# Performance work log

Hardware: AMD Instinct MI355X
Metric: run time of the kernel (lower is better)

## Reference

```python
import jax, jax.numpy as jnp
import numpy as np

B, C, N = 4, 128, 25000
E = 200000            # edges per graph
H, DH = 4, 32         # heads, per-head dim
OUT = H * DH          # 128
ED = 32               # edge feature dim


def setup_inputs() -> dict:
    key = jax.random.key(0)
    ks = jax.random.split(key, 16)
    s = 0.05
    return {
        'x': jax.random.normal(ks[0], (B, C, N, 1), jnp.float32),
        'edge_index': jax.random.randint(ks[1], (B, 2, E), 0, B * N, jnp.int64),
        'edge_attr': jax.random.normal(ks[2], (B * E, ED), jnp.float32),
        'Wq': jax.random.normal(ks[3], (C, OUT), jnp.float32) * s,
        'bq': jnp.zeros((OUT,), jnp.float32),
        'Wk': jax.random.normal(ks[4], (C, OUT), jnp.float32) * s,
        'bk': jnp.zeros((OUT,), jnp.float32),
        'Wv': jax.random.normal(ks[5], (C, OUT), jnp.float32) * s,
        'bv': jnp.zeros((OUT,), jnp.float32),
        'We': jax.random.normal(ks[6], (ED, OUT), jnp.float32) * s,
        'Wskip': jax.random.normal(ks[7], (C, OUT), jnp.float32) * s,
        'bskip': jnp.zeros((OUT,), jnp.float32),
        'W1': jax.random.normal(ks[8], (OUT, 2 * OUT), jnp.float32) * s,
        'b1': jnp.zeros((2 * OUT,), jnp.float32),
        'W2': jax.random.normal(ks[9], (2 * OUT, OUT), jnp.float32) * s,
        'b2': jnp.zeros((OUT,), jnp.float32),
    }


def reference(x, edge_index, edge_attr, Wq, bq, Wk, bk, Wv, bv, We,
              Wskip, bskip, W1, b1, W2, b2):
    b, c, n, _ = x.shape
    nb = b * n
    # [B,C,N,1] -> [B*N, C]
    xf = x.squeeze(-1).transpose(0, 2, 1).reshape(nb, c)
    # [B,2,E] -> [2, B*E]
    ei = edge_index.transpose(1, 0, 2).reshape(2, -1)
    src, dst = ei[0], ei[1]

    q = (xf @ Wq + bq).reshape(nb, H, DH)
    k = (xf @ Wk + bk).reshape(nb, H, DH)
    v = (xf @ Wv + bv).reshape(nb, H, DH)
    e = (edge_attr @ We).reshape(-1, H, DH)  # [T,H,DH]

    qi = q[dst]            # gather target queries  [T,H,DH]
    kj = k[src] + e        # gather source keys + edge proj
    vj = v[src] + e

    scale = 1.0 / np.sqrt(DH).astype(np.float32)
    alpha = (qi * kj).sum(-1) * scale  # [T,H]

    # segment softmax over edges sharing a destination node
    amax = jax.ops.segment_max(alpha, dst, num_segments=nb)
    amax = jnp.where(jnp.isfinite(amax), amax, 0.0)
    ea = jnp.exp(alpha - amax[dst])
    denom = jax.ops.segment_sum(ea, dst, num_segments=nb)
    attn = ea / (denom[dst] + 1e-16)   # [T,H]

    agg = jax.ops.segment_sum(vj * attn[..., None], dst, num_segments=nb)
    out = agg.reshape(nb, OUT) + (xf @ Wskip + bskip)  # root skip

    # feed-forward + final activation
    h = jnp.maximum(out @ W1 + b1, 0.0) @ W2 + b2
    h = jnp.maximum(h, 0.0)

    # [B*N, OUT] -> [B, OUT, N, 1]
    return h.reshape(b, n, OUT).transpose(0, 2, 1)[..., None]
```

## Files before the change

### kernel.cpp

```cpp
#include <hip/hip_runtime.h>
#include <hip/hip_bf16.h>

#define NB      100000
#define NPB     25000
#define T_E     800000
#define EPG     200000
#define DMODEL  128
#define EDIM    32
#define FFD     256
#define SCAN_NBLK 98

typedef __attribute__((ext_vector_type(8))) short bf16x8;
typedef __attribute__((ext_vector_type(4))) float f32x4;
typedef __attribute__((ext_vector_type(2))) float f32x2;

__device__ inline unsigned short f2bf(float f) {
    unsigned u = __float_as_uint(f);
    unsigned r = u + 0x7fffu + ((u >> 16) & 1u);
    return (unsigned short)(r >> 16);
}
__device__ inline unsigned pack_bf16x2(float lo, float hi) {
    return (unsigned)f2bf(lo) | ((unsigned)f2bf(hi) << 16);
}
__device__ inline float bf_lo(unsigned p) { return __uint_as_float(p << 16); }
__device__ inline float bf_hi(unsigned p) { return __uint_as_float(p & 0xffff0000u); }

__global__ __launch_bounds__(256) void k_prep(
    const float* __restrict__ W1, const float* __restrict__ W2,
    const float* __restrict__ We,
    const float* __restrict__ Wq, const float* __restrict__ Wk,
    const float* __restrict__ Wv, const float* __restrict__ Wskip,
    uint4* __restrict__ w1f, uint4* __restrict__ w2f,
    uint4* __restrict__ wef, uint4* __restrict__ wpf)
{
    int t = blockIdx.x * 256 + threadIdx.x;
    int lane = t & 63;
    int frag = t >> 6;
    if (frag >= 264) return;
    int rl = lane & 15, g = lane >> 4;
    unsigned v[4];
    if (frag < 64) {
        int m1 = frag >> 2, ks = frag & 3;
        int col1 = m1 * 16 + rl;
        int k0 = ks * 32 + g * 8;
#pragma unroll
        for (int j2 = 0; j2 < 4; ++j2) {
            float f0 = W1[(k0 + 2 * j2) * FFD + col1];
            float f1 = W1[(k0 + 2 * j2 + 1) * FFD + col1];
            v[j2] = pack_bf16x2(f0, f1);
        }
        w1f[frag * 64 + lane] = make_uint4(v[0], v[1], v[2], v[3]);
    } else if (frag < 128) {
        int f2 = frag - 64;
        int m2 = f2 >> 3, ks = f2 & 7;
        int c2 = m2 * 16 + rl;
        int k0 = ks * 32 + g * 8;
#pragma unroll
        for (int j2 = 0; j2 < 4; ++j2) {
            float f0 = W2[(k0 + 2 * j2) * DMODEL + c2];
            float f1 = W2[(k0 + 2 * j2 + 1) * DMODEL + c2];
            v[j2] = pack_bf16x2(f0, f1);
        }
        w2f[f2 * 64 + lane] = make_uint4(v[0], v[1], v[2], v[3]);
    } else if (frag < 136) {
        int m = frag - 128;
        int ocol = m * 16 + rl;
        int k0 = g * 8;
#pragma unroll
        for (int j2 = 0; j2 < 4; ++j2) {
            float f0 = We[(k0 + 2 * j2) * DMODEL + ocol];
            float f1 = We[(k0 + 2 * j2 + 1) * DMODEL + ocol];
            v[j2] = pack_bf16x2(f0, f1);
        }
        wef[m * 64 + lane] = make_uint4(v[0], v[1], v[2], v[3]);
    } else {
        int fi = frag - 136;
        int m  = fi >> 5;
        int r  = fi & 31;
        int ct = r >> 2, ks = r & 3;
        const float* W = (m == 0) ? Wq : (m == 1) ? Wk : (m == 2) ? Wv : Wskip;
        int col = ct * 16 + rl;
        int k0  = ks * 32 + g * 8;
#pragma unroll
        for (int j2 = 0; j2 < 4; ++j2) {
            float f0 = W[(k0 + 2 * j2) * DMODEL + col];
            float f1 = W[(k0 + 2 * j2 + 1) * DMODEL + col];
            v[j2] = pack_bf16x2(f0, f1);
        }
        wpf[fi * 64 + lane] = make_uint4(v[0], v[1], v[2], v[3]);
    }
}

__global__ __launch_bounds__(256) void k_proj2(
    const float* __restrict__ x, const uint4* __restrict__ wpf,
    const float* __restrict__ bq, const float* __restrict__ bk,
    const float* __restrict__ bv, const float* __restrict__ bskip,
    unsigned short* __restrict__ qb16, unsigned short* __restrict__ kvb,
    unsigned short* __restrict__ skipb16)
{
    __shared__ __align__(16) char lds[16384];
    const int tid   = threadIdx.x;
    const int node0 = blockIdx.x * 64;

    {
        const int nl   = tid & 63;
        const int half = tid >> 6;
        const int node = node0 + nl;
        const bool valid = node < NB;
        int b  = node / NPB;
        int nn = node - b * NPB;
        const float* xbase = x + (size_t)b * DMODEL * NPB + nn;
#pragma unroll
        for (int o = 0; o < 4; ++o) {
            int c0 = (half * 4 + o) * 8;
            unsigned vals[4];
#pragma unroll
            for (int j2 = 0; j2 < 4; ++j2) {
                float f0 = valid ? xbase[(size_t)(c0 + 2 * j2) * NPB] : 0.f;
                float f1 = valid ? xbase[(size_t)(c0 + 2 * j2 + 1) * NPB] : 0.f;
                vals[j2] = pack_bf16x2(f0, f1);
            }
            int byte = nl * 256 + ((c0 * 2) ^ ((nl & 7) << 4));
            *(uint4*)(&lds[byte]) = make_uint4(vals[0], vals[1], vals[2], vals[3]);
        }
    }
    __syncthreads();

    const int w = tid >> 6, lane = tid & 63;
    const int rl = lane & 15, g = lane >> 4;

    const uint4* wf = wpf + (size_t)w * 32 * 64;
    const float* bi = (w == 0) ? bq : (w == 1) ? bk : (w == 2) ? bv : bskip;
    unsigned short* base = (w == 0) ? qb16 : (w == 3) ? skipb16
                          : kvb + ((w == 2) ? 128 : 0);
    const int rowstride = (w == 1 || w == 2) ? 256 : 128;

#pragma unroll
    for (int ct = 0; ct < 8; ++ct) {
        bf16x8 A[4];
#pragma unroll
        for (int ks = 0; ks < 4; ++ks)
            A[ks] = *(const bf16x8*)&wf[(ct * 4 + ks) * 64 + lane];
        const int colb = ct * 16 + g * 4;
        const float bb0 = bi[colb], bb1 = bi[colb + 1],
                    bb2 = bi[colb + 2], bb3 = bi[colb + 3];
#pragma unroll
        for (int nt = 0; nt < 4; ++nt) {
            const int nl = nt * 16 + rl;
            f32x4 acc = {0.f, 0.f, 0.f, 0.f};
#pragma unroll
            for (int ks = 0; ks < 4; ++ks) {
                bf16x8 B = *(const bf16x8*)(&lds[nl * 256 +
                              ((ks * 64 + g * 16) ^ ((nl & 7) << 4))]);
                acc = __builtin_amdgcn_mfma_f32_16x16x32_bf16(A[ks], B, acc, 0, 0, 0);
            }
            const int node = node0 + nl;
            if (node < NB) {
                unsigned lo = pack_bf16x2(acc[0] + bb0, acc[1] + bb1);
                unsigned hi = pack_bf16x2(acc[2] + bb2, acc[3] + bb3);
                *(uint2*)&base[(size_t)node * rowstride + colb] = make_uint2(lo, hi);
            }
        }
    }
}

__global__ __launch_bounds__(256) void k_hist(
    const int* __restrict__ eidx, int* __restrict__ counts)
{
    int t = blockIdx.x * 256 + threadIdx.x;
    if (t < T_E) {
        int b = t / EPG, e = t - b * EPG;
        int dst = eidx[(size_t)(b * 2 + 1) * EPG + e];
        atomicAdd(&counts[dst], 1);
    }
}

__global__ __launch_bounds__(1024) void k_scan1(
    const int* __restrict__ counts, int* __restrict__ row_start,
    int* __restrict__ bsum)
{
    __shared__ int s[1024];
    const int tid = threadIdx.x;
    const int gid = blockIdx.x * 1024 + tid;
    int v = (gid < NB) ? counts[gid] : 0;
    s[tid] = v;
    __syncthreads();
#pragma unroll
    for (int off = 1; off < 1024; off <<= 1) {
        int tv = (tid >= off) ? s[tid - off] : 0;
        __syncthreads();
        s[tid] += tv;
        __syncthreads();
    }
    int incl = s[tid];
    if (gid < NB) row_start[gid] = incl - v;
    if (tid == 1023) bsum[blockIdx.x] = incl;
}

__global__ __launch_bounds__(128) void k_scan2(int* __restrict__ bsum)
{
    __shared__ int s[128];
    const int tid = threadIdx.x;
    int v = (tid < SCAN_NBLK) ? bsum[tid] : 0;
    s[tid] = v;
    __syncthreads();
#pragma unroll
    for (int off = 1; off < 128; off <<= 1) {
        int tv = (tid >= off) ? s[tid - off] : 0;
        __syncthreads();
        s[tid] += tv;
        __syncthreads();
    }
    if (tid < SCAN_NBLK) bsum[tid] = s[tid] - v;
}

__global__ __launch_bounds__(1024) void k_scan3(
    int* __restrict__ row_start, const int* __restrict__ bsum,
    int* __restrict__ cursor)
{
    const int gid = blockIdx.x * 1024 + threadIdx.x;
    if (gid < NB) {
        int v = row_start[gid] + bsum[blockIdx.x];
        row_start[gid] = v;
        cursor[gid] = v;
    }
}

__global__ __launch_bounds__(256) void k_scatter(
    const int* __restrict__ eidx, int* __restrict__ cursor,
    int2* __restrict__ elist2)
{
    int t = blockIdx.x * 256 + threadIdx.x;
    if (t < T_E) {
        int b = t / EPG, e = t - b * EPG;
        int dst = eidx[(size_t)(b * 2 + 1) * EPG + e];
        int src = eidx[(size_t)(b * 2) * EPG + e];
        int pos = atomicAdd(&cursor[dst], 1);
        elist2[pos] = make_int2(src, t);
    }
}

__global__ __launch_bounds__(256) void k_eproj(
    const float* __restrict__ eattr, const uint4* __restrict__ wef,
    unsigned char* __restrict__ eb)
{
    const int tid = threadIdx.x;
    const int w = tid >> 6, lane = tid & 63;
    const int rl = lane & 15, g = lane >> 4;

    bf16x8 a[8];
#pragma unroll
    for (int m = 0; m < 8; ++m) a[m] = *(const bf16x8*)&wef[m * 64 + lane];

    const int nwaves = gridDim.x * 4;
    for (int tile = blockIdx.x * 4 + w; tile < T_E / 16; tile += nwaves) {
        const float* ep = &eattr[((size_t)tile * 16 + rl) * EDIM + g * 8];
        float4 f0 = *(const float4*)ep;
        float4 f1 = *(const float4*)(ep + 4);
        uint4 bu = make_uint4(pack_bf16x2(f0.x, f0.y), pack_bf16x2(f0.z, f0.w),
                              pack_bf16x2(f1.x, f1.y), pack_bf16x2(f1.z, f1.w));
        bf16x8 b = *(bf16x8*)&bu;
        f32x4 z = {0.f, 0.f, 0.f, 0.f};
        f32x4 acc[8];
#pragma unroll
        for (int m = 0; m < 8; ++m)
            acc[m] = __builtin_amdgcn_mfma_f32_16x16x32_bf16(a[m], b, z, 0, 0, 0);
        unsigned char* out = &eb[((size_t)tile * 16 + rl) * DMODEL + g * 4];
#pragma unroll
        for (int m = 0; m < 8; ++m) {
            unsigned d = __builtin_amdgcn_cvt_pk_fp8_f32(acc[m][0], acc[m][1], 0, false);
            d = __builtin_amdgcn_cvt_pk_fp8_f32(acc[m][2], acc[m][3], d, true);
            *(unsigned*)(out + m * 16) = d;
        }
    }
}

__global__ __launch_bounds__(256) void k_aggr3(
    unsigned short* qx,
    const unsigned short* __restrict__ kvb,
    const unsigned short* __restrict__ skipb16,
    const unsigned char* __restrict__ eb,
    const int2* __restrict__ elist2,
    const int* __restrict__ row_start, const int* __restrict__ row_end)
{
    const int tid = threadIdx.x;
    const int w = tid >> 6, l = tid & 63;
    const int q4 = l >> 4;
    const int li = l & 15;
    const int c0 = li * 8;

    const int nwaves = gridDim.x * 4;
    for (int node = blockIdx.x * 4 + w; node < NB; node += nwaves) {
        const int rs = row_start[node];
        const int re = row_end[node];
        uint4 qp = *(const uint4*)&qx[(size_t)node * DMODEL + c0];
        const float q0 = bf_lo(qp.x), q1 = bf_hi(qp.x);
        const float q2 = bf_lo(qp.y), q3 = bf_hi(qp.y);
        const float q4_ = bf_lo(qp.z), q5 = bf_hi(qp.z);
        const float q6 = bf_lo(qp.w), q7 = bf_hi(qp.w);
        float a0 = 0.f, a1 = 0.f, a2 = 0.f, a3 = 0.f;
        float a4 = 0.f, a5 = 0.f, a6 = 0.f, a7 = 0.f, den = 0.f;

        for (int j0 = rs; j0 < re; j0 += 4) {
            const int jc = j0 + q4;
            const bool act = jc < re;
            uint4 kp = make_uint4(0, 0, 0, 0), vp = make_uint4(0, 0, 0, 0);
            uint2 ep8 = make_uint2(0, 0);
            if (act) {
                int2 se = elist2[jc];
                kp = *(const uint4*)&kvb[(size_t)se.x * 256 + c0];
                vp = *(const uint4*)&kvb[(size_t)se.x * 256 + 128 + c0];
                ep8 = *(const uint2*)&eb[(size_t)se.y * DMODEL + c0];
            }
            f32x2 exl = __builtin_amdgcn_cvt_pk_f32_fp8(ep8.x, false);
            f32x2 exh = __builtin_amdgcn_cvt_pk_f32_fp8(ep8.x, true);
            f32x2 eyl = __builtin_amdgcn_cvt_pk_f32_fp8(ep8.y, false);
            f32x2 eyh = __builtin_amdgcn_cvt_pk_f32_fp8(ep8.y, true);
            const float e0 = exl[0], e1 = exl[1], e2 = exh[0], e3 = exh[1];
            const float e4 = eyl[0], e5 = eyl[1], e6 = eyh[0], e7 = eyh[1];
            const float k0 = bf_lo(kp.x) + e0, k1 = bf_hi(kp.x) + e1;
            const float k2 = bf_lo(kp.y) + e2, k3 = bf_hi(kp.y) + e3;
            const float k4 = bf_lo(kp.z) + e4, k5 = bf_hi(kp.z) + e5;
            const float k6 = bf_lo(kp.w) + e6, k7 = bf_hi(kp.w) + e7;
            float p = q0 * k0 + q1 * k1 + q2 * k2 + q3 * k3
                    + q4_ * k4 + q5 * k5 + q6 * k6 + q7 * k7;
            p += __shfl_xor(p, 1, 64);
            p += __shfl_xor(p, 2, 64);
            float ea = act ? __expf(p * 0.17677669529663689f) : 0.f;
            a0 += ea * (bf_lo(vp.x) + e0);
            a1 += ea * (bf_hi(vp.x) + e1);
            a2 += ea * (bf_lo(vp.y) + e2);
            a3 += ea * (bf_hi(vp.y) + e3);
            a4 += ea * (bf_lo(vp.z) + e4);
            a5 += ea * (bf_hi(vp.z) + e5);
            a6 += ea * (bf_lo(vp.w) + e6);
            a7 += ea * (bf_hi(vp.w) + e7);
            den += ea;
        }
#pragma unroll
        for (int off = 16; off <= 32; off <<= 1) {
            a0 += __shfl_xor(a0, off, 64);
            a1 += __shfl_xor(a1, off, 64);
            a2 += __shfl_xor(a2, off, 64);
            a3 += __shfl_xor(a3, off, 64);
            a4 += __shfl_xor(a4, off, 64);
            a5 += __shfl_xor(a5, off, 64);
            a6 += __shfl_xor(a6, off, 64);
            a7 += __shfl_xor(a7, off, 64);
            den += __shfl_xor(den, off, 64);
        }
        float r = 1.0f / (den + 1e-16f);
        if (q4 == 0) {
            uint4 sp = *(const uint4*)&skipb16[(size_t)node * DMODEL + c0];
            uint4 o;
            o.x = pack_bf16x2(a0 * r + bf_lo(sp.x), a1 * r + bf_hi(sp.x));
            o.y = pack_bf16x2(a2 * r + bf_lo(sp.y), a3 * r + bf_hi(sp.y));
            o.z = pack_bf16x2(a4 * r + bf_lo(sp.z), a5 * r + bf_hi(sp.z));
            o.w = pack_bf16x2(a6 * r + bf_lo(sp.w), a7 * r + bf_hi(sp.w));
            *(uint4*)&qx[(size_t)node * DMODEL + c0] = o;
        }
    }
}

#define H1_OFF 16384

__global__ __launch_bounds__(256) void k_ffn_mfma(
    const unsigned short* __restrict__ xs16,
    const uint4* __restrict__ w1f, const float* __restrict__ b1,
    const uint4* __restrict__ w2f, const float* __restrict__ b2,
    float* __restrict__ out)
{
    __shared__ __align__(16) char lds[49152];
    const int tid   = threadIdx.x;
    const int node0 = blockIdx.x * 64;

#pragma unroll
    for (int i = 0; i < 4; ++i) {
        int linear = i * 256 + tid;
        int row = linear >> 4;
        int c8  = (linear & 15) * 8;
        int node = node0 + row;
        uint4 vv = (node < NB) ? *(const uint4*)&xs16[(size_t)node * DMODEL + c8]
                               : make_uint4(0, 0, 0, 0);
        int byte = row * 256 + ((c8 * 2) ^ ((row & 7) << 4));
        *(uint4*)(&lds[byte]) = vv;
    }
    __syncthreads();

    const int w = tid >> 6, lane = tid & 63;
    const int rl = lane & 15, g = lane >> 4;

    {
        f32x4 acc[4][4] = {};
#pragma unroll
        for (int ks = 0; ks < 4; ++ks) {
            bf16x8 a[4], b[4];
#pragma unroll
            for (int mt = 0; mt < 4; ++mt) {
                int m1 = w * 4 + mt;
                a[mt] = *(const bf16x8*)&w1f[(m1 * 4 + ks) * 64 + lane];
            }
#pragma unroll
            for (int nt = 0; nt < 4; ++nt) {
                int node = nt * 16 + rl;
                int byte = node * 256 + ((ks * 64 + g * 16) ^ ((node & 7) << 4));
                b[nt] = *(const bf16x8*)&lds[byte];
            }
#pragma unroll
            for (int mt = 0; mt < 4; ++mt)
#pragma unroll
                for (int nt = 0; nt < 4; ++nt)
                    acc[mt][nt] = __builtin_amdgcn_mfma_f32_16x16x32_bf16(
                        a[mt], b[nt], acc[mt][nt], 0, 0, 0);
        }
#pragma unroll
        for (int mt = 0; mt < 4; ++mt) {
            int col1_0 = w * 64 + mt * 16 + g * 4;
            float bb0 = b1[col1_0], bb1 = b1[col1_0 + 1],
                  bb2 = b1[col1_0 + 2], bb3 = b1[col1_0 + 3];
#pragma unroll
            for (int nt = 0; nt < 4; ++nt) {
                int node = nt * 16 + rl;
                float v0 = fmaxf(acc[mt][nt][0] + bb0, 0.f);
                float v1 = fmaxf(acc[mt][nt][1] + bb1, 0.f);
                float v2 = fmaxf(acc[mt][nt][2] + bb2, 0.f);
                float v3 = fmaxf(acc[mt][nt][3] + bb3, 0.f);
                unsigned lo = pack_bf16x2(v0, v1), hi = pack_bf16x2(v2, v3);
                int byte = H1_OFF + node * 512 + ((col1_0 * 2) ^ ((node & 7) << 4));
                *(uint2*)(&lds[byte]) = make_uint2(lo, hi);
            }
        }
    }
    __syncthreads();

    {
        f32x4 acc[2][4] = {};
#pragma unroll
        for (int ks = 0; ks < 8; ++ks) {
            bf16x8 a[2], b[4];
#pragma unroll
            for (int mt = 0; mt < 2; ++mt) {
                int m2 = w * 2 + mt;
                a[mt] = *(const bf16x8*)&w2f[(m2 * 8 + ks) * 64 + lane];
            }
#pragma unroll
            for (int nt = 0; nt < 4; ++nt) {
                int node = nt * 16 + rl;
                int byte = H1_OFF + node * 512 + ((ks * 64 + g * 16) ^ ((node & 7) << 4));
                b[nt] = *(const bf16x8*)&lds[byte];
            }
#pragma unroll
            for (int mt = 0; mt < 2; ++mt)
#pragma unroll
                for (int nt = 0; nt < 4; ++nt)
                    acc[mt][nt] = __builtin_amdgcn_mfma_f32_16x16x32_bf16(
                        a[mt], b[nt], acc[mt][nt], 0, 0, 0);
        }
#pragma unroll
        for (int mt = 0; mt < 2; ++mt) {
            int c2_0 = w * 32 + mt * 16 + g * 4;
#pragma unroll
            for (int nt = 0; nt < 4; ++nt) {
                int node = node0 + nt * 16 + rl;
                if (node < NB) {
                    int bb = node / NPB;
                    int nn = node - bb * NPB;
                    size_t base = (size_t)(bb * DMODEL) * NPB + nn;
#pragma unroll
                    for (int r = 0; r < 4; ++r) {
                        float v = fmaxf(acc[mt][nt][r] + b2[c2_0 + r], 0.f);
                        out[base + (size_t)(c2_0 + r) * NPB] = v;
                    }
                }
            }
        }
    }
}

extern "C" void kernel_launch(void* const* d_in, const int* in_sizes, int n_in,
                              void* d_out, int out_size, void* d_ws, size_t ws_size,
                              hipStream_t stream)
{
    const float* x     = (const float*)d_in[0];
    const int*   eidx  = (const int*)  d_in[1];
    const float* eattr = (const float*)d_in[2];
    const float* Wq    = (const float*)d_in[3];
    const float* bq    = (const float*)d_in[4];
    const float* Wk    = (const float*)d_in[5];
    const float* bk    = (const float*)d_in[6];
    const float* Wv    = (const float*)d_in[7];
    const float* bv    = (const float*)d_in[8];
    const float* We    = (const float*)d_in[9];
    const float* Wskip = (const float*)d_in[10];
    const float* bskip = (const float*)d_in[11];
    const float* W1    = (const float*)d_in[12];
    const float* b1    = (const float*)d_in[13];
    const float* W2    = (const float*)d_in[14];
    const float* b2    = (const float*)d_in[15];
    float* out = (float*)d_out;

    const size_t NBD = (size_t)NB * DMODEL;
    unsigned short* qb16    = (unsigned short*)d_ws;
    unsigned short* kvb     = qb16 + NBD;
    unsigned short* skipb16 = kvb + 2 * NBD;
    unsigned char*  eb      = (unsigned char*)(skipb16 + NBD);
    uint4* w1f = (uint4*)(eb + (size_t)T_E * DMODEL);
    uint4* w2f = w1f + 64 * 64;
    uint4* wef = w2f + 64 * 64;
    uint4* wpf = wef + 8 * 64;
    int* counts    = (int*)(wpf + 128 * 64);
    int* row_start = counts + NB;
    int* cursor    = row_start + NB;
    int2* elist2   = (int2*)(cursor + NB);
    int* bsum      = (int*)(elist2 + T_E);

    hipMemsetAsync(counts, 0, NB * sizeof(int), stream);
    k_prep<<<66, 256, 0, stream>>>(W1, W2, We, Wq, Wk, Wv, Wskip,
                                   w1f, w2f, wef, wpf);
    k_proj2<<<(NB + 63) / 64, 256, 0, stream>>>(x, wpf, bq, bk, bv, bskip,
                                                qb16, kvb, skipb16);
    k_hist<<<(T_E + 255) / 256, 256, 0, stream>>>(eidx, counts);
    k_scan1<<<SCAN_NBLK, 1024, 0, stream>>>(counts, row_start, bsum);
    k_scan2<<<1, 128, 0, stream>>>(bsum);
    k_scan3<<<SCAN_NBLK, 1024, 0, stream>>>(row_start, bsum, cursor);
    k_scatter<<<(T_E + 255) / 256, 256, 0, stream>>>(eidx, cursor, elist2);
    k_eproj<<<2048, 256, 0, stream>>>(eattr, wef, eb);
    k_aggr3<<<2048, 256, 0, stream>>>(qb16, kvb, skipb16, eb, elist2,
                                      row_start, cursor);
    k_ffn_mfma<<<(NB + 63) / 64, 256, 0, stream>>>(qb16, w1f, b1, w2f, b2, out);
}
```

Before: 369.1 us.

## Eliminate per-edge projection by folding We into query and aggregated edge sums

Removes the k_eproj kernel that materialised an fp8 projected edge tensor for every edge. Instead q·(We e) is computed as (We^T q)·e with a per-node qe vector precomputed in k_proj2, and the attention-weighted sum of raw edge attributes is accumulated per node and projected through a block-diagonal We in the FFN kernel. k_proj2 now stages its outputs through LDS so global writes are coalesced. The cost is extra per-node buffers and MFMA work, plus reading fp32 edge attributes (32 floats per edge) gathered by edge id inside the aggregation loop.

```diff
diff --git a/kernel.cpp b/kernel.cpp
--- a/kernel.cpp
+++ b/kernel.cpp
@@ -12,7 +12,6 @@
 
 typedef __attribute__((ext_vector_type(8))) short bf16x8;
 typedef __attribute__((ext_vector_type(4))) float f32x4;
-typedef __attribute__((ext_vector_type(2))) float f32x2;
 
 __device__ inline unsigned short f2bf(float f) {
     unsigned u = __float_as_uint(f);
@@ -31,12 +30,12 @@
     const float* __restrict__ Wq, const float* __restrict__ Wk,
     const float* __restrict__ Wv, const float* __restrict__ Wskip,
     uint4* __restrict__ w1f, uint4* __restrict__ w2f,
-    uint4* __restrict__ wef, uint4* __restrict__ wpf)
+    uint4* __restrict__ wpf, uint4* __restrict__ wbdf, uint4* __restrict__ wetf)
 {
     int t = blockIdx.x * 256 + threadIdx.x;
     int lane = t & 63;
     int frag = t >> 6;
-    if (frag >= 264) return;
+    if (frag >= 320) return;
     int rl = lane & 15, g = lane >> 4;
     unsigned v[4];
     if (frag < 64) {
@@ -62,19 +61,8 @@
             v[j2] = pack_bf16x2(f0, f1);
         }
         w2f[f2 * 64 + lane] = make_uint4(v[0], v[1], v[2], v[3]);
-    } else if (frag < 136) {
-        int m = frag - 128;
-        int ocol = m * 16 + rl;
-        int k0 = g * 8;
-#pragma unroll
-        for (int j2 = 0; j2 < 4; ++j2) {
-            float f0 = We[(k0 + 2 * j2) * DMODEL + ocol];
-            float f1 = We[(k0 + 2 * j2 + 1) * DMODEL + ocol];
-            v[j2] = pack_bf16x2(f0, f1);
-        }
-        wef[m * 64 + lane] = make_uint4(v[0], v[1], v[2], v[3]);
-    } else {
-        int fi = frag - 136;
+    } else if (frag < 256) {
+        int fi = frag - 128;
         int m  = fi >> 5;
         int r  = fi & 31;
         int ct = r >> 2, ks = r & 3;
@@ -88,17 +76,46 @@
             v[j2] = pack_bf16x2(f0, f1);
         }
         wpf[fi * 64 + lane] = make_uint4(v[0], v[1], v[2], v[3]);
-    }
-}
+    } else if (frag < 288) {
+        int fi = frag - 256;
+        int ct = fi >> 2, ks = fi & 3;
+        int c = ct * 16 + rl;
+        int k0 = ks * 32 + g * 8;
+#pragma unroll
+        for (int j2 = 0; j2 < 4; ++j2) {
+            int ka = k0 + 2 * j2, kb = k0 + 2 * j2 + 1;
+            float f0 = ((ka >> 5) == (c >> 5)) ? We[(ka & 31) * DMODEL + c] : 0.f;
+            float f1 = ((kb >> 5) == (c >> 5)) ? We[(kb & 31) * DMODEL + c] : 0.f;
+            v[j2] = pack_bf16x2(f0, f1);
+        }
+        wbdf[fi * 64 + lane] = make_uint4(v[0], v[1], v[2], v[3]);
+    } else {
+        int fi = frag - 288;
+        int ct = fi >> 2, ks = fi & 3;
+        int c = ct * 16 + rl;
+        int k0 = ks * 32 + g * 8;
+#pragma unroll
+        for (int j2 = 0; j2 < 4; ++j2) {
+            int ka = k0 + 2 * j2, kb = k0 + 2 * j2 + 1;
+            float f0 = ((ka >> 5) == (c >> 5)) ? We[(c & 31) * DMODEL + ka] : 0.f;
+            float f1 = ((kb >> 5) == (c >> 5)) ? We[(c & 31) * DMODEL + kb] : 0.f;
+            v[j2] = pack_bf16x2(f0, f1);
+        }
+        wetf[fi * 64 + lane] = make_uint4(v[0], v[1], v[2], v[3]);
+    }
+}
+
+#define STG 16384
 
 __global__ __launch_bounds__(256) void k_proj2(
     const float* __restrict__ x, const uint4* __restrict__ wpf,
+    const uint4* __restrict__ wetf,
     const float* __restrict__ bq, const float* __restrict__ bk,
     const float* __restrict__ bv, const float* __restrict__ bskip,
     unsigned short* __restrict__ qb16, unsigned short* __restrict__ kvb,
-    unsigned short* __restrict__ skipb16)
-{
-    __shared__ __align__(16) char lds[16384];
+    unsigned short* __restrict__ skipb16, unsigned short* __restrict__ qeh16)
+{
+    __shared__ __align__(16) char lds[32768];
     const int tid   = threadIdx.x;
     const int node0 = blockIdx.x * 64;
 
@@ -129,37 +146,92 @@
     const int w = tid >> 6, lane = tid & 63;
     const int rl = lane & 15, g = lane >> 4;
 
-    const uint4* wf = wpf + (size_t)w * 32 * 64;
-    const float* bi = (w == 0) ? bq : (w == 1) ? bk : (w == 2) ? bv : bskip;
-    unsigned short* base = (w == 0) ? qb16 : (w == 3) ? skipb16
-                          : kvb + ((w == 2) ? 128 : 0);
-    const int rowstride = (w == 1 || w == 2) ? 256 : 128;
-
-#pragma unroll
-    for (int ct = 0; ct < 8; ++ct) {
-        bf16x8 A[4];
-#pragma unroll
-        for (int ks = 0; ks < 4; ++ks)
-            A[ks] = *(const bf16x8*)&wf[(ct * 4 + ks) * 64 + lane];
-        const int colb = ct * 16 + g * 4;
-        const float bb0 = bi[colb], bb1 = bi[colb + 1],
-                    bb2 = bi[colb + 2], bb3 = bi[colb + 3];
-#pragma unroll
-        for (int nt = 0; nt < 4; ++nt) {
-            const int nl = nt * 16 + rl;
-            f32x4 acc = {0.f, 0.f, 0.f, 0.f};
-#pragma unroll
-            for (int ks = 0; ks < 4; ++ks) {
-                bf16x8 B = *(const bf16x8*)(&lds[nl * 256 +
-                              ((ks * 64 + g * 16) ^ ((nl & 7) << 4))]);
-                acc = __builtin_amdgcn_mfma_f32_16x16x32_bf16(A[ks], B, acc, 0, 0, 0);
-            }
-            const int node = node0 + nl;
-            if (node < NB) {
+    for (int m = 0; m < 4; ++m) {
+        const float* bi = (m == 0) ? bq : (m == 1) ? bk : (m == 2) ? bv : bskip;
+#pragma unroll
+        for (int ct2 = 0; ct2 < 2; ++ct2) {
+            const int ct = w * 2 + ct2;
+            bf16x8 A[4];
+#pragma unroll
+            for (int ks = 0; ks < 4; ++ks)
+                A[ks] = *(const bf16x8*)&wpf[((m * 8 + ct) * 4 + ks) * 64 + lane];
+            const int colb = ct * 16 + g * 4;
+            const float bb0 = bi[colb], bb1 = bi[colb + 1],
+                        bb2 = bi[colb + 2], bb3 = bi[colb + 3];
+#pragma unroll
+            for (int nt = 0; nt < 4; ++nt) {
+                const int nl = nt * 16 + rl;
+                f32x4 acc = {0.f, 0.f, 0.f, 0.f};
+#pragma unroll
+                for (int ks = 0; ks < 4; ++ks) {
+                    bf16x8 B = *(const bf16x8*)(&lds[nl * 256 +
+                                  ((ks * 64 + g * 16) ^ ((nl & 7) << 4))]);
+                    acc = __builtin_amdgcn_mfma_f32_16x16x32_bf16(A[ks], B, acc, 0, 0, 0);
+                }
                 unsigned lo = pack_bf16x2(acc[0] + bb0, acc[1] + bb1);
                 unsigned hi = pack_bf16x2(acc[2] + bb2, acc[3] + bb3);
-                *(uint2*)&base[(size_t)node * rowstride + colb] = make_uint2(lo, hi);
-            }
+                int byte = STG + nl * 256 + ((colb * 2) ^ ((nl & 7) << 4));
+                *(uint2*)(&lds[byte]) = make_uint2(lo, hi);
+            }
+        }
+        __syncthreads();
+#pragma unroll
+        for (int i = 0; i < 4; ++i) {
+            int linear = i * 256 + tid;
+            int row = linear >> 4;
+            int c8  = (linear & 15) * 8;
+            int node = node0 + row;
+            if (node < NB) {
+                uint4 vv = *(const uint4*)(&lds[STG + row * 256 +
+                                ((c8 * 2) ^ ((row & 7) << 4))]);
+                if (m == 0)      *(uint4*)&qb16[(size_t)node * DMODEL + c8] = vv;
+                else if (m == 1) *(uint4*)&kvb[(size_t)node * 256 + c8] = vv;
+                else if (m == 2) *(uint4*)&kvb[(size_t)node * 256 + 128 + c8] = vv;
+                else             *(uint4*)&skipb16[(size_t)node * DMODEL + c8] = vv;
+            }
+        }
+        __syncthreads();
+
+        if (m == 0) {
+            f32x4 qacc[8] = {};
+            bf16x8 QA[4];
+            const int arow = w * 16 + rl;
+#pragma unroll
+            for (int ks = 0; ks < 4; ++ks)
+                QA[ks] = *(const bf16x8*)(&lds[STG + arow * 256 +
+                              ((ks * 64 + g * 16) ^ ((arow & 7) << 4))]);
+#pragma unroll
+            for (int ks = 0; ks < 4; ++ks)
+#pragma unroll
+                for (int ct = 0; ct < 8; ++ct) {
+                    bf16x8 b = *(const bf16x8*)&wetf[(ct * 4 + ks) * 64 + lane];
+                    qacc[ct] = __builtin_amdgcn_mfma_f32_16x16x32_bf16(QA[ks], b, qacc[ct], 0, 0, 0);
+                }
+            __syncthreads();
+#pragma unroll
+            for (int ct = 0; ct < 8; ++ct) {
+                const int col = ct * 16 + rl;
+#pragma unroll
+                for (int r = 0; r < 4; ++r) {
+                    const int nl = w * 16 + g * 4 + r;
+                    int byte = STG + nl * 256 + ((col * 2) ^ ((nl & 7) << 4));
+                    *(unsigned short*)(&lds[byte]) = f2bf(qacc[ct][r]);
+                }
+            }
+            __syncthreads();
+#pragma unroll
+            for (int i = 0; i < 4; ++i) {
+                int linear = i * 256 + tid;
+                int row = linear >> 4;
+                int c8  = (linear & 15) * 8;
+                int node = node0 + row;
+                if (node < NB) {
+                    uint4 vv = *(const uint4*)(&lds[STG + row * 256 +
+                                    ((c8 * 2) ^ ((row & 7) << 4))]);
+                    *(uint4*)&qeh16[(size_t)node * DMODEL + c8] = vv;
+                }
+            }
+            __syncthreads();
         }
     }
 }
@@ -240,46 +312,13 @@
     }
 }
 
-__global__ __launch_bounds__(256) void k_eproj(
-    const float* __restrict__ eattr, const uint4* __restrict__ wef,
-    unsigned char* __restrict__ eb)
-{
-    const int tid = threadIdx.x;
-    const int w = tid >> 6, lane = tid & 63;
-    const int rl = lane & 15, g = lane >> 4;
-
-    bf16x8 a[8];
-#pragma unroll
-    for (int m = 0; m < 8; ++m) a[m] = *(const bf16x8*)&wef[m * 64 + lane];
-
-    const int nwaves = gridDim.x * 4;
-    for (int tile = blockIdx.x * 4 + w; tile < T_E / 16; tile += nwaves) {
-        const float* ep = &eattr[((size_t)tile * 16 + rl) * EDIM + g * 8];
-        float4 f0 = *(const float4*)ep;
-        float4 f1 = *(const float4*)(ep + 4);
-        uint4 bu = make_uint4(pack_bf16x2(f0.x, f0.y), pack_bf16x2(f0.z, f0.w),
-                              pack_bf16x2(f1.x, f1.y), pack_bf16x2(f1.z, f1.w));
-        bf16x8 b = *(bf16x8*)&bu;
-        f32x4 z = {0.f, 0.f, 0.f, 0.f};
-        f32x4 acc[8];
-#pragma unroll
-        for (int m = 0; m < 8; ++m)
-            acc[m] = __builtin_amdgcn_mfma_f32_16x16x32_bf16(a[m], b, z, 0, 0, 0);
-        unsigned char* out = &eb[((size_t)tile * 16 + rl) * DMODEL + g * 4];
-#pragma unroll
-        for (int m = 0; m < 8; ++m) {
-            unsigned d = __builtin_amdgcn_cvt_pk_fp8_f32(acc[m][0], acc[m][1], 0, false);
-            d = __builtin_amdgcn_cvt_pk_fp8_f32(acc[m][2], acc[m][3], d, true);
-            *(unsigned*)(out + m * 16) = d;
-        }
-    }
-}
-
 __global__ __launch_bounds__(256) void k_aggr3(
     unsigned short* qx,
     const unsigned short* __restrict__ kvb,
     const unsigned short* __restrict__ skipb16,
-    const unsigned char* __restrict__ eb,
+    const unsigned short* __restrict__ qeh16,
+    const float* __restrict__ eattr,
+    unsigned short* __restrict__ se16,
     const int2* __restrict__ elist2,
     const int* __restrict__ row_start, const int* __restrict__ row_end)
 {
@@ -288,65 +327,68 @@
     const int q4 = l >> 4;
     const int li = l & 15;
     const int c0 = li * 8;
+    const int ed0 = (li & 3) * 8;
 
     const int nwaves = gridDim.x * 4;
     for (int node = blockIdx.x * 4 + w; node < NB; node += nwaves) {
         const int rs = row_start[node];
         const int re = row_end[node];
-        uint4 qp = *(const uint4*)&qx[(size_t)node * DMODEL + c0];
+        uint4 qp  = *(const uint4*)&qx[(size_t)node * DMODEL + c0];
+        uint4 qep = *(const uint4*)&qeh16[(size_t)node * DMODEL + c0];
         const float q0 = bf_lo(qp.x), q1 = bf_hi(qp.x);
         const float q2 = bf_lo(qp.y), q3 = bf_hi(qp.y);
         const float q4_ = bf_lo(qp.z), q5 = bf_hi(qp.z);
         const float q6 = bf_lo(qp.w), q7 = bf_hi(qp.w);
+        const float qe0 = bf_lo(qep.x), qe1 = bf_hi(qep.x);
+        const float qe2 = bf_lo(qep.y), qe3 = bf_hi(qep.y);
+        const float qe4 = bf_lo(qep.z), qe5 = bf_hi(qep.z);
+        const float qe6 = bf_lo(qep.w), qe7 = bf_hi(qep.w);
         float a0 = 0.f, a1 = 0.f, a2 = 0.f, a3 = 0.f;
-        float a4 = 0.f, a5 = 0.f, a6 = 0.f, a7 = 0.f, den = 0.f;
+        float a4 = 0.f, a5 = 0.f, a6 = 0.f, a7 = 0.f;
+        float s0 = 0.f, s1 = 0.f, s2 = 0.f, s3 = 0.f;
+        float s4 = 0.f, s5 = 0.f, s6 = 0.f, s7 = 0.f, den = 0.f;
 
         for (int j0 = rs; j0 < re; j0 += 4) {
             const int jc = j0 + q4;
             const bool act = jc < re;
             uint4 kp = make_uint4(0, 0, 0, 0), vp = make_uint4(0, 0, 0, 0);
-            uint2 ep8 = make_uint2(0, 0);
+            float4 ef0 = make_float4(0.f, 0.f, 0.f, 0.f);
+            float4 ef1 = make_float4(0.f, 0.f, 0.f, 0.f);
             if (act) {
                 int2 se = elist2[jc];
                 kp = *(const uint4*)&kvb[(size_t)se.x * 256 + c0];
                 vp = *(const uint4*)&kvb[(size_t)se.x * 256 + 128 + c0];
-                ep8 = *(const uint2*)&eb[(size_t)se.y * DMODEL + c0];
-            }
-            f32x2 exl = __builtin_amdgcn_cvt_pk_f32_fp8(ep8.x, false);
-            f32x2 exh = __builtin_amdgcn_cvt_pk_f32_fp8(ep8.x, true);
-            f32x2 eyl = __builtin_amdgcn_cvt_pk_f32_fp8(ep8.y, false);
-            f32x2 eyh = __builtin_amdgcn_cvt_pk_f32_fp8(ep8.y, true);
-            const float e0 = exl[0], e1 = exl[1], e2 = exh[0], e3 = exh[1];
-            const float e4 = eyl[0], e5 = eyl[1], e6 = eyh[0], e7 = eyh[1];
-            const float k0 = bf_lo(kp.x) + e0, k1 = bf_hi(kp.x) + e1;
-            const float k2 = bf_lo(kp.y) + e2, k3 = bf_hi(kp.y) + e3;
-            const float k4 = bf_lo(kp.z) + e4, k5 = bf_hi(kp.z) + e5;
-            const float k6 = bf_lo(kp.w) + e6, k7 = bf_hi(kp.w) + e7;
-            float p = q0 * k0 + q1 * k1 + q2 * k2 + q3 * k3
-                    + q4_ * k4 + q5 * k5 + q6 * k6 + q7 * k7;
+                const float* ep = &eattr[(size_t)se.y * EDIM + ed0];
+                ef0 = *(const float4*)ep;
+                ef1 = *(const float4*)(ep + 4);
+            }
+            float p = q0 * bf_lo(kp.x) + q1 * bf_hi(kp.x)
+                    + q2 * bf_lo(kp.y) + q3 * bf_hi(kp.y)
+                    + q4_ * bf_lo(kp.z) + q5 * bf_hi(kp.z)
+                    + q6 * bf_lo(kp.w) + q7 * bf_hi(kp.w)
+                    + qe0 * ef0.x + qe1 * ef0.y + qe2 * ef0.z + qe3 * ef0.w
+                    + qe4 * ef1.x + qe5 * ef1.y + qe6 * ef1.z + qe7 * ef1.w;
             p += __shfl_xor(p, 1, 64);
             p += __shfl_xor(p, 2, 64);
             float ea = act ? __expf(p * 0.17677669529663689f) : 0.f;
-            a0 += ea * (bf_lo(vp.x) + e0);
-            a1 += ea * (bf_hi(vp.x) + e1);
-            a2 += ea * (bf_lo(vp.y) + e2);
-            a3 += ea * (bf_hi(vp.y) + e3);
-            a4 += ea * (bf_lo(vp.z) + e4);
-            a5 += ea * (bf_hi(vp.z) + e5);
-            a6 += ea * (bf_lo(vp.w) + e6);
-            a7 += ea * (bf_hi(vp.w) + e7);
+            a0 += ea * bf_lo(vp.x);  a1 += ea * bf_hi(vp.x);
+            a2 += ea * bf_lo(vp.y);  a3 += ea * bf_hi(vp.y);
+            a4 += ea * bf_lo(vp.z);  a5 += ea * bf_hi(vp.z);
+            a6 += ea * bf_lo(vp.w);  a7 += ea * bf_hi(vp.w);
+            s0 += ea * ef0.x;  s1 += ea * ef0.y;  s2 += ea * ef0.z;  s3 += ea * ef0.w;
+            s4 += ea * ef1.x;  s5 += ea * ef1.y;  s6 += ea * ef1.z;  s7 += ea * ef1.w;
             den += ea;
         }
 #pragma unroll
         for (int off = 16; off <= 32; off <<= 1) {
-            a0 += __shfl_xor(a0, off, 64);
-            a1 += __shfl_xor(a1, off, 64);
-            a2 += __shfl_xor(a2, off, 64);
-            a3 += __shfl_xor(a3, off, 64);
-            a4 += __shfl_xor(a4, off, 64);
-            a5 += __shfl_xor(a5, off, 64);
-            a6 += __shfl_xor(a6, off, 64);
-            a7 += __shfl_xor(a7, off, 64);
+            a0 += __shfl_xor(a0, off, 64);  a1 += __shfl_xor(a1, off, 64);
+            a2 += __shfl_xor(a2, off, 64);  a3 += __shfl_xor(a3, off, 64);
+            a4 += __shfl_xor(a4, off, 64);  a5 += __shfl_xor(a5, off, 64);
+            a6 += __shfl_xor(a6, off, 64);  a7 += __shfl_xor(a7, off, 64);
+            s0 += __shfl_xor(s0, off, 64);  s1 += __shfl_xor(s1, off, 64);
+            s2 += __shfl_xor(s2, off, 64);  s3 += __shfl_xor(s3, off, 64);
+            s4 += __shfl_xor(s4, off, 64);  s5 += __shfl_xor(s5, off, 64);
+            s6 += __shfl_xor(s6, off, 64);  s7 += __shfl_xor(s7, off, 64);
             den += __shfl_xor(den, off, 64);
         }
         float r = 1.0f / (den + 1e-16f);
@@ -358,6 +400,12 @@
             o.z = pack_bf16x2(a4 * r + bf_lo(sp.z), a5 * r + bf_hi(sp.z));
             o.w = pack_bf16x2(a6 * r + bf_lo(sp.w), a7 * r + bf_hi(sp.w));
             *(uint4*)&qx[(size_t)node * DMODEL + c0] = o;
+            uint4 so;
+            so.x = pack_bf16x2(s0 * r, s1 * r);
+            so.y = pack_bf16x2(s2 * r, s3 * r);
+            so.z = pack_bf16x2(s4 * r, s5 * r);
+            so.w = pack_bf16x2(s6 * r, s7 * r);
+            *(uint4*)&se16[(size_t)node * DMODEL + c0] = so;
         }
     }
 }
@@ -366,8 +414,10 @@
 
 __global__ __launch_bounds__(256) void k_ffn_mfma(
     const unsigned short* __restrict__ xs16,
+    const unsigned short* __restrict__ se16,
     const uint4* __restrict__ w1f, const float* __restrict__ b1,
     const uint4* __restrict__ w2f, const float* __restrict__ b2,
+    const uint4* __restrict__ wbdf,
     float* __restrict__ out)
 {
     __shared__ __align__(16) char lds[49152];
@@ -380,15 +430,48 @@
         int row = linear >> 4;
         int c8  = (linear & 15) * 8;
         int node = node0 + row;
-        uint4 vv = (node < NB) ? *(const uint4*)&xs16[(size_t)node * DMODEL + c8]
+        uint4 xv = (node < NB) ? *(const uint4*)&xs16[(size_t)node * DMODEL + c8]
                                : make_uint4(0, 0, 0, 0);
-        int byte = row * 256 + ((c8 * 2) ^ ((row & 7) << 4));
-        *(uint4*)(&lds[byte]) = vv;
+        uint4 sv = (node < NB) ? *(const uint4*)&se16[(size_t)node * DMODEL + c8]
+                               : make_uint4(0, 0, 0, 0);
+        int off = row * 256 + ((c8 * 2) ^ ((row & 7) << 4));
+        *(uint4*)(&lds[off]) = xv;
+        *(uint4*)(&lds[H1_OFF + off]) = sv;
     }
     __syncthreads();
 
     const int w = tid >> 6, lane = tid & 63;
     const int rl = lane & 15, g = lane >> 4;
+
+    {
+        f32x4 acc0[8] = {};
+        bf16x8 A0[4];
+        const int arow = w * 16 + rl;
+#pragma unroll
+        for (int ks = 0; ks < 4; ++ks)
+            A0[ks] = *(const bf16x8*)(&lds[H1_OFF + arow * 256 +
+                          ((ks * 64 + g * 16) ^ ((arow & 7) << 4))]);
+#pragma unroll
+        for (int ks = 0; ks < 4; ++ks)
+#pragma unroll
+            for (int ct = 0; ct < 8; ++ct) {
+                bf16x8 b = *(const bf16x8*)&wbdf[(ct * 4 + ks) * 64 + lane];
+                acc0[ct] = __builtin_amdgcn_mfma_f32_16x16x32_bf16(A0[ks], b, acc0[ct], 0, 0, 0);
+            }
+#pragma unroll
+        for (int ct = 0; ct < 8; ++ct) {
+            const int col = ct * 16 + rl;
+#pragma unroll
+            for (int r = 0; r < 4; ++r) {
+                const int nl = w * 16 + g * 4 + r;
+                int byte = nl * 256 + ((col * 2) ^ ((nl & 7) << 4));
+                unsigned short* p = (unsigned short*)&lds[byte];
+                float xv = __uint_as_float(((unsigned)*p) << 16);
+                *p = f2bf(xv + acc0[ct][r]);
+            }
+        }
+    }
+    __syncthreads();
 
     {
         f32x4 acc[4][4] = {};
@@ -503,29 +586,31 @@
     unsigned short* qb16    = (unsigned short*)d_ws;
     unsigned short* kvb     = qb16 + NBD;
     unsigned short* skipb16 = kvb + 2 * NBD;
-    unsigned char*  eb      = (unsigned char*)(skipb16 + NBD);
-    uint4* w1f = (uint4*)(eb + (size_t)T_E * DMODEL);
-    uint4* w2f = w1f + 64 * 64;
-    uint4* wef = w2f + 64 * 64;
-    uint4* wpf = wef + 8 * 64;
-    int* counts    = (int*)(wpf + 128 * 64);
+    unsigned short* qeh16   = skipb16 + NBD;
+    unsigned short* se16    = qeh16 + NBD;
+    uint4* w1f  = (uint4*)(se16 + NBD);
+    uint4* w2f  = w1f + 64 * 64;
+    uint4* wpf  = w2f + 64 * 64;
+    uint4* wbdf = wpf + 128 * 64;
+    uint4* wetf = wbdf + 32 * 64;
+    int* counts    = (int*)(wetf + 32 * 64);
     int* row_start = counts + NB;
     int* cursor    = row_start + NB;
     int2* elist2   = (int2*)(cursor + NB);
     int* bsum      = (int*)(elist2 + T_E);
 
     hipMemsetAsync(counts, 0, NB * sizeof(int), stream);
-    k_prep<<<66, 256, 0, stream>>>(W1, W2, We, Wq, Wk, Wv, Wskip,
-                                   w1f, w2f, wef, wpf);
-    k_proj2<<<(NB + 63) / 64, 256, 0, stream>>>(x, wpf, bq, bk, bv, bskip,
-                                                qb16, kvb, skipb16);
+    k_prep<<<80, 256, 0, stream>>>(W1, W2, We, Wq, Wk, Wv, Wskip,
+                                   w1f, w2f, wpf, wbdf, wetf);
+    k_proj2<<<(NB + 63) / 64, 256, 0, stream>>>(x, wpf, wetf, bq, bk, bv, bskip,
+                                                qb16, kvb, skipb16, qeh16);
     k_hist<<<(T_E + 255) / 256, 256, 0, stream>>>(eidx, counts);
     k_scan1<<<SCAN_NBLK, 1024, 0, stream>>>(counts, row_start, bsum);
     k_scan2<<<1, 128, 0, stream>>>(bsum);
     k_scan3<<<SCAN_NBLK, 1024, 0, stream>>>(row_start, bsum, cursor);
     k_scatter<<<(T_E + 255) / 256, 256, 0, stream>>>(eidx, cursor, elist2);
-    k_eproj<<<2048, 256, 0, stream>>>(eattr, wef, eb);
-    k_aggr3<<<2048, 256, 0, stream>>>(qb16, kvb, skipb16, eb, elist2,
-                                      row_start, cursor);
-    k_ffn_mfma<<<(NB + 63) / 64, 256, 0, stream>>>(qb16, w1f, b1, w2f, b2, out);
-}
+    k_aggr3<<<2048, 256, 0, stream>>>(qb16, kvb, skipb16, qeh16, eattr, se16,
+                                      elist2, row_start, cursor);
+    k_ffn_mfma<<<(NB + 63) / 64, 256, 0, stream>>>(qb16, se16, w1f, b1, w2f, b2,
+                                                   wbdf, out);
+}
```

Result: no change. 363.6 us (-1.5%).
